# Kernel optimization log

Hardware: AMD Instinct MI355X
Metric: run time of the kernel (lower is better)

The kernel has to match this reference:

```python
import jax, jax.numpy as jnp
import numpy as np

N, F, E, WID, M, K = 100000, 128, 128, 4, 25000, 16
HID = WID * F    # width * num_features = 512
DHID = WID * E   # discriminator hidden = 512
EPS = 1e-5


def _v2v(x, v_idx, w_e):
    """Hypergraph v2v mean aggregation: v->e mean (scaled by w_e), then e->v mean."""
    Mm, Kk = v_idx.shape
    C = x.shape[1]
    ef = jnp.zeros((Mm, C), x.dtype)
    for k in range(Kk):  # K is small and static; avoids a [M,K,C] materialization
        ef = ef + x[v_idx[:, k]]
    ef = ef * (w_e / Kk)[:, None]  # weighted edge features [M, C]
    out = jnp.zeros_like(x)
    deg = jnp.zeros((x.shape[0],), x.dtype)
    for k in range(Kk):
        out = out.at[v_idx[:, k]].add(ef)
        deg = deg.at[v_idx[:, k]].add(1.0)
    return out / jnp.maximum(deg, 1.0)[:, None]


def _bn(h, g, bt):
    # BatchNorm1d in training mode: biased batch stats over vertex dim
    m = h.mean(0)
    v = ((h - m) ** 2).mean(0)
    return g * (h - m) * jax.lax.rsqrt(v + EPS) + bt


def _conv(x, Wt, b, g, bt, v_idx, w_e, last=False):
    h = _bn(x @ Wt.T + b, g, bt)
    h = _v2v(h, v_idx, w_e)
    return h if last else jax.nn.relu(h)  # dropout = identity (eval mode)


def setup_inputs() -> dict:
    key = jax.random.key(0)
    ks = iter(jax.random.split(key, 64))

    def lin(o, i):
        s = 1.0 / np.sqrt(i)
        return (jax.random.uniform(next(ks), (o, i), minval=-s, maxval=s, dtype=jnp.float32),
                jax.random.uniform(next(ks), (o,), minval=-s, maxval=s, dtype=jnp.float32))

    d = {}
    d["X"] = jax.random.normal(next(ks), (N, F), dtype=jnp.float32)
    d["v_idx"] = jax.random.randint(next(ks), (M, K), 0, N, dtype=jnp.int32)
    d["w_e"] = jax.random.uniform(next(ks), (M,), dtype=jnp.float32)
    for name, (o, i) in [("enc1", (HID, F)), ("enc2", (E, HID)), ("fc", (E, HID)),
                         ("f1u", (E, E)), ("f2u", (E, E)), ("f1r", (E, E)), ("f2r", (E, E)),
                         ("f1", (E, E)), ("f2", (E, E)),
                         ("dis1", (DHID, E)), ("dis2", (2, DHID)),
                         ("dec1", (HID, E)), ("dec2", (F, HID))]:
        Wt, b = lin(o, i)
        d[name + "_W"] = Wt
        d[name + "_b"] = b
    for name, c in [("enc1", HID), ("enc2", E), ("dis1", DHID), ("dis2", 2), ("dec1", HID), ("dec2", F)]:
        d[name + "_g"] = jnp.ones((c,), jnp.float32)
        d[name + "_bt"] = jnp.zeros((c,), jnp.float32)
    return d


def reference(X, v_idx, w_e,
              enc1_W, enc1_b, enc2_W, enc2_b, fc_W, fc_b,
              f1u_W, f1u_b, f2u_W, f2u_b, f1r_W, f1r_b, f2r_W, f2r_b,
              f1_W, f1_b, f2_W, f2_b,
              dis1_W, dis1_b, dis2_W, dis2_b, dec1_W, dec1_b, dec2_W, dec2_b,
              enc1_g, enc1_bt, enc2_g, enc2_bt, dis1_g, dis1_bt, dis2_g, dis2_bt,
              dec1_g, dec1_bt, dec2_g, dec2_bt):
    # encoder (returns last output and first-layer output)
    x1 = _conv(X, enc1_W, enc1_b, enc1_g, enc1_bt, v_idx, w_e)            # [N, HID]
    xe = _conv(x1, enc2_W, enc2_b, enc2_g, enc2_bt, v_idx, w_e, last=True)  # [N, E]
    xe1 = x1 @ fc_W.T + fc_b                                               # [N, E]
    # GRU-style gating
    z = jax.nn.sigmoid(xe1 @ f1u_W.T + f1u_b + xe @ f2u_W.T + f2u_b)
    r = jax.nn.sigmoid(xe1 @ f1r_W.T + f1r_b + xe @ f2r_W.T + f2r_b)
    o = jnp.tanh(xe1 @ f1_W.T + f1_b + (r * xe) @ f2_W.T + f2_b)
    outs = z * o + (1.0 - z) * xe                                          # [N, E]
    # attention pooling (n = input_size - 1)
    dd = (outs - outs.mean(0)) ** 2
    vv = dd.sum(0) / (N - 1)
    ee = dd / (4.0 * (vv + 0.001)) + 0.5
    proto = (outs * jax.nn.sigmoid(ee)).sum(0)                             # [E]
    # gradient reversal is identity in the forward pass
    h = _conv(outs, dis1_W, dis1_b, dis1_g, dis1_bt, v_idx, w_e)
    xdis = _conv(h, dis2_W, dis2_b, dis2_g, dis2_bt, v_idx, w_e, last=True)  # [N, 2]
    h = _conv(outs, dec1_W, dec1_b, dec1_g, dec1_bt, v_idx, w_e)
    x_de = _conv(h, dec2_W, dec2_b, dec2_g, dec2_bt, v_idx, w_e, last=True)  # [N, F]
    return (outs, x_de, proto, xdis)
```

## Files before the change

kernel.cpp:

```cpp
#include <hip/hip_runtime.h>
#include <cstddef>
#include <cstdint>

static constexpr int NV = 100000;
static constexpr int NP = 100096;
static constexpr int ME = 25000;
static constexpr int MEP = 25088;
static constexpr int KE = 16;
static constexpr float BN_EPS = 1e-5f;

typedef unsigned int u32;
typedef __attribute__((ext_vector_type(8))) short s16x8;
typedef __attribute__((ext_vector_type(8))) unsigned short u16x8;
typedef __attribute__((ext_vector_type(4))) float f32x4;

__device__ __forceinline__ float sigm(float x) { return 1.0f / (1.0f + expf(-x)); }
__device__ __forceinline__ float bf2f(unsigned short u) {
    union { u32 i; float f; } v; v.i = ((u32)u) << 16; return v.f;
}
__device__ __forceinline__ unsigned short f2bf(float f) {
    union { float f; u32 i; } v; v.f = f;
    u32 u = v.i;
    return (unsigned short)((u + 0x7FFFu + ((u >> 16) & 1u)) >> 16);
}

#define GLD16(g, l) __builtin_amdgcn_global_load_lds(                          \
    (__attribute__((address_space(1))) const unsigned int*)(g),                \
    (__attribute__((address_space(3))) unsigned int*)(l), 16, 0, 0)

#define STAGE_AB(b, k0)                                                        \
  {                                                                            \
    unsigned short* sA_ = sm + (b) * 12288;                                    \
    unsigned short* sB_ = sA_ + 8192;                                          \
    _Pragma("unroll")                                                          \
    for (int i_ = 0; i_ < 4; ++i_) {                                           \
      const unsigned short* g_ = A + (size_t)(bm + 32 * w + 8 * i_ + (l >> 3)) * IC + (k0) + swz; \
      GLD16(g_, sA_ + 2048 * w + 512 * i_);                                    \
    }                                                                          \
    _Pragma("unroll")                                                          \
    for (int i_ = 0; i_ < 2; ++i_) {                                           \
      const unsigned short* g_ = W + (size_t)(bn + 16 * w + 8 * i_ + (l >> 3)) * IC + (k0) + swz; \
      GLD16(g_, sB_ + 1024 * w + 512 * i_);                                    \
    }                                                                          \
  }

__global__ __launch_bounds__(256)
void mfma_gemm(const unsigned short* __restrict__ A, int IC,
               const unsigned short* __restrict__ W, const float* __restrict__ bias,
               unsigned short* __restrict__ Cb, int ldb, int cb0,
               unsigned short* __restrict__ Cb2, int ldb2, int splitN,
               float* __restrict__ s1f, float* __restrict__ s2f, int statsC)
{
    __shared__ unsigned short sm[2 * 12288];
    const int bm = blockIdx.y * 128;
    const int bn = blockIdx.x * 64;
    const int tid = threadIdx.x;
    const int l = tid & 63, w = tid >> 6;
    const int wrow = w >> 1, wcol = w & 1;

    f32x4 acc[4][2];
    #pragma unroll
    for (int m = 0; m < 4; ++m)
        #pragma unroll
        for (int n = 0; n < 2; ++n)
            #pragma unroll
            for (int r = 0; r < 4; ++r) acc[m][n][r] = 0.f;

    const int swz = (((l & 7) ^ (l >> 3)) << 3);
    const int nt = IC >> 6;

    STAGE_AB(0, 0);
    asm volatile("s_waitcnt vmcnt(0)" ::: "memory");
    __builtin_amdgcn_s_barrier();

    for (int t = 0; t < nt; ++t) {
        const int cur = t & 1;
        if (t + 1 < nt) STAGE_AB(cur ^ 1, (t + 1) << 6);
        const unsigned short* sA = sm + cur * 12288;
        const unsigned short* sB = sA + 8192;
        #pragma unroll
        for (int ks = 0; ks < 2; ++ks) {
            const int koff = ks * 32 + ((l >> 4) << 3);
            s16x8 afr[4], bfr[2];
            #pragma unroll
            for (int m = 0; m < 4; ++m) {
                int row = wrow * 64 + m * 16 + (l & 15);
                afr[m] = *(const s16x8*)&sA[row * 64 + (koff ^ ((l & 7) << 3))];
            }
            #pragma unroll
            for (int n = 0; n < 2; ++n) {
                int col = wcol * 32 + n * 16 + (l & 15);
                bfr[n] = *(const s16x8*)&sB[col * 64 + (koff ^ ((l & 7) << 3))];
            }
            #pragma unroll
            for (int m = 0; m < 4; ++m)
                #pragma unroll
                for (int n = 0; n < 2; ++n)
                    acc[m][n] = __builtin_amdgcn_mfma_f32_16x16x32_bf16(
                        afr[m], bfr[n], acc[m][n], 0, 0, 0);
        }
        asm volatile("s_waitcnt vmcnt(0)" ::: "memory");
        __builtin_amdgcn_s_barrier();
    }

    unsigned short* dst = Cb;
    int ld = ldb, co = cb0;
    if (Cb2 && bn >= splitN) { dst = Cb2; ld = ldb2; co = -splitN; }

    #pragma unroll
    for (int n = 0; n < 2; ++n) {
        const int col = bn + wcol * 32 + n * 16 + (l & 15);
        const float bs = bias[col];
        float ssum = 0.f, sq = 0.f;
        #pragma unroll
        for (int m = 0; m < 4; ++m) {
            const int row0 = bm + wrow * 64 + m * 16 + ((l >> 4) << 2);
            #pragma unroll
            for (int r = 0; r < 4; ++r) {
                float v = acc[m][n][r] + bs;
                int row = row0 + r;
                if (dst) dst[(size_t)row * ld + co + col] = f2bf(v);
                if (s1f && col < statsC && row < NV) { ssum += v; sq += v * v; }
            }
        }
        if (s1f && col < statsC) {
            ssum += __shfl_xor(ssum, 16); ssum += __shfl_xor(ssum, 32);
            sq   += __shfl_xor(sq, 16);   sq   += __shfl_xor(sq, 32);
            if ((l >> 4) == 0) {
                atomicAdd(&s1f[col], ssum);
                atomicAdd(&s2f[col], sq);
            }
        }
    }
}

__global__ __launch_bounds__(256)
void mfma_gemm_vtx(const unsigned short* __restrict__ A,
                   const unsigned short* __restrict__ W,
                   const float* __restrict__ P, const float* __restrict__ Q,
                   const float* __restrict__ sw,
                   unsigned short* __restrict__ dst, int ldd, int colStart,
                   const unsigned short* __restrict__ disW,
                   float* __restrict__ pre22)
{
    const int IC = 128;
    __shared__ unsigned short sm[2 * 12288];
    const int bm = blockIdx.y * 128;
    const int bn = blockIdx.x * 64;
    const int tid = threadIdx.x;
    const int l = tid & 63, w = tid >> 6;
    const int wrow = w >> 1, wcol = w & 1;

    f32x4 acc[4][2];
    #pragma unroll
    for (int m = 0; m < 4; ++m)
        #pragma unroll
        for (int n = 0; n < 2; ++n)
            #pragma unroll
            for (int r = 0; r < 4; ++r) acc[m][n][r] = 0.f;

    const int swz = (((l & 7) ^ (l >> 3)) << 3);

    STAGE_AB(0, 0);
    asm volatile("s_waitcnt vmcnt(0)" ::: "memory");
    __builtin_amdgcn_s_barrier();

    #pragma unroll
    for (int t = 0; t < 2; ++t) {
        const int cur = t & 1;
        if (t == 0) STAGE_AB(1, 64);
        const unsigned short* sA = sm + cur * 12288;
        const unsigned short* sB = sA + 8192;
        #pragma unroll
        for (int ks = 0; ks < 2; ++ks) {
            const int koff = ks * 32 + ((l >> 4) << 3);
            s16x8 afr[4], bfr[2];
            #pragma unroll
            for (int m = 0; m < 4; ++m) {
                int row = wrow * 64 + m * 16 + (l & 15);
                afr[m] = *(const s16x8*)&sA[row * 64 + (koff ^ ((l & 7) << 3))];
            }
            #pragma unroll
            for (int n = 0; n < 2; ++n) {
                int col = wcol * 32 + n * 16 + (l & 15);
                bfr[n] = *(const s16x8*)&sB[col * 64 + (koff ^ ((l & 7) << 3))];
            }
            #pragma unroll
            for (int m = 0; m < 4; ++m)
                #pragma unroll
                for (int n = 0; n < 2; ++n)
                    acc[m][n] = __builtin_amdgcn_mfma_f32_16x16x32_bf16(
                        afr[m], bfr[n], acc[m][n], 0, 0, 0);
        }
        asm volatile("s_waitcnt vmcnt(0)" ::: "memory");
        __builtin_amdgcn_s_barrier();
    }

    if (disW && bn < colStart) {
        #pragma unroll
        for (int m = 0; m < 4; ++m) {
            #pragma unroll
            for (int r = 0; r < 4; ++r) {
                const int row = bm + wrow * 64 + m * 16 + ((l >> 4) << 2) + r;
                const float swr = sw[row];
                float p0 = 0.f, p1 = 0.f;
                #pragma unroll
                for (int n = 0; n < 2; ++n) {
                    const int col = bn + wcol * 32 + n * 16 + (l & 15);
                    float h = fmaxf(P[col] * acc[m][n][r] + swr * Q[col], 0.f);
                    p0 += h * bf2f(disW[col]);
                    p1 += h * bf2f(disW[512 + col]);
                }
                p0 += __shfl_xor(p0, 1); p0 += __shfl_xor(p0, 2);
                p0 += __shfl_xor(p0, 4); p0 += __shfl_xor(p0, 8);
                p1 += __shfl_xor(p1, 1); p1 += __shfl_xor(p1, 2);
                p1 += __shfl_xor(p1, 4); p1 += __shfl_xor(p1, 8);
                if ((l & 15) == 0 && row < NV) {
                    atomicAdd(&pre22[2 * row], p0);
                    atomicAdd(&pre22[2 * row + 1], p1);
                }
            }
        }
    } else {
        #pragma unroll
        for (int n = 0; n < 2; ++n) {
            const int col = bn + wcol * 32 + n * 16 + (l & 15);
            const float pc = P[col], qc = Q[col];
            #pragma unroll
            for (int m = 0; m < 4; ++m) {
                const int row0 = bm + wrow * 64 + m * 16 + ((l >> 4) << 2);
                #pragma unroll
                for (int r = 0; r < 4; ++r) {
                    const int row = row0 + r;
                    float h = fmaxf(pc * acc[m][n][r] + sw[row] * qc, 0.f);
                    dst[(size_t)row * ldd + col - colStart] = f2bf(h);
                }
            }
        }
    }
}

__global__ __launch_bounds__(256)
void cov_kernel(const unsigned short* __restrict__ A, float* __restrict__ cov)
{
    __shared__ unsigned short T[128 * 64];
    const int tid = threadIdx.x;
    const int l = tid & 63, w = tid >> 6;

    f32x4 acc[2][8];
    #pragma unroll
    for (int m = 0; m < 2; ++m)
        #pragma unroll
        for (int n = 0; n < 8; ++n)
            #pragma unroll
            for (int r = 0; r < 4; ++r) acc[m][n][r] = 0.f;

    const int r0 = blockIdx.x * 1024;
    for (int ch = 0; ch < 16; ++ch) {
        const int rbase = r0 + ch * 64;
        __syncthreads();
        #pragma unroll
        for (int q = 0; q < 4; ++q) {
            int idx = tid + q * 256;
            int r = idx & 63, cg = idx >> 6;
            int row = rbase + r;
            u16x8 u = {0, 0, 0, 0, 0, 0, 0, 0};
            if (row < NV) u = *(const u16x8*)&A[(size_t)row * 128 + cg * 8];
            #pragma unroll
            for (int j = 0; j < 8; ++j) {
                int c = cg * 8 + j;
                T[c * 64 + (r ^ ((c & 7) << 3))] = u[j];
            }
        }
        __syncthreads();
        #pragma unroll
        for (int ks = 0; ks < 2; ++ks) {
            const int koff = ks * 32 + ((l >> 4) << 3);
            s16x8 fi[2], fj[8];
            #pragma unroll
            for (int m = 0; m < 2; ++m) {
                int c = (w * 2 + m) * 16 + (l & 15);
                fi[m] = *(const s16x8*)&T[c * 64 + (koff ^ ((c & 7) << 3))];
            }
            #pragma unroll
            for (int n = 0; n < 8; ++n) {
                int c = n * 16 + (l & 15);
                fj[n] = *(const s16x8*)&T[c * 64 + (koff ^ ((c & 7) << 3))];
            }
            #pragma unroll
            for (int m = 0; m < 2; ++m)
                #pragma unroll
                for (int n = 0; n < 8; ++n)
                    acc[m][n] = __builtin_amdgcn_mfma_f32_16x16x32_bf16(
                        fi[m], fj[n], acc[m][n], 0, 0, 0);
        }
    }
    #pragma unroll
    for (int m = 0; m < 2; ++m) {
        #pragma unroll
        for (int n = 0; n < 8; ++n) {
            #pragma unroll
            for (int r = 0; r < 4; ++r) {
                int row = (w * 2 + m) * 16 + ((l >> 4) << 2) + r;
                int col = n * 16 + (l & 15);
                atomicAdd(&cov[row * 128 + col], acc[m][n][r]);
            }
        }
    }
}

__global__ __launch_bounds__(128)
void quadform_kernel(const float* __restrict__ cov, const float* __restrict__ colsum,
                     const unsigned short* __restrict__ Wt, const float* __restrict__ bias,
                     float* __restrict__ s1, float* __restrict__ s2)
{
    const int c = blockIdx.x, i = threadIdx.x;
    __shared__ float wv[128];
    __shared__ float red[128][2];
    float wi = bf2f(Wt[c * 128 + i]);
    wv[i] = wi;
    __syncthreads();
    const float* crow = cov + i * 128;
    float dot = 0.f;
    #pragma unroll 8
    for (int j = 0; j < 128; ++j) dot += crow[j] * wv[j];
    red[i][0] = wi * dot;
    red[i][1] = wi * colsum[i];
    __syncthreads();
    for (int s = 64; s > 0; s >>= 1) {
        if (i < s) { red[i][0] += red[i + s][0]; red[i][1] += red[i + s][1]; }
        __syncthreads();
    }
    if (i == 0) {
        float b = bias[c];
        float ws = red[0][1];
        s1[c] = ws + (float)NV * b;
        s2[c] = red[0][0] + 2.f * b * ws + (float)NV * b * b;
    }
}

__global__ void prep_weights(const float* e1, const float* e2, const float* fcw,
                             const float* d1, const float* dc1, const float* dc2,
                             const float* ds2,
                             const float* f1u, const float* f2u,
                             const float* f1r, const float* f2r,
                             const float* f1, const float* f2,
                             const float* f1ub, const float* f2ub,
                             const float* f1rb, const float* f2rb,
                             const float* f1b, const float* f2b,
                             const float* ds1b, const float* dc1b,
                             const float* e2b, const float* fcb,
                             unsigned short* WB, float* bzr, float* bo,
                             float* bdd, float* bef)
{
    int i = blockIdx.x * 256 + threadIdx.x;
    if (i < 65536)           WB[i] = f2bf(e1[i]);
    else if (i < 131072)     WB[i] = f2bf(e2[i - 65536]);
    else if (i < 196608)     WB[i] = f2bf(fcw[i - 131072]);
    else if (i < 262144)     WB[i] = f2bf(d1[i - 196608]);
    else if (i < 327680)     WB[i] = f2bf(dc1[i - 262144]);
    else if (i < 393216)     WB[i] = f2bf(dc2[i - 327680]);
    else if (i < 394240)     WB[i] = f2bf(ds2[i - 393216]);
    else if (i < 459776) {
        int j = i - 394240, row = j >> 8, c = j & 255;
        float v;
        if (row < 128) v = (c < 128) ? f1u[row * 128 + c] : f2u[row * 128 + c - 128];
        else { int rr = row - 128; v = (c < 128) ? f1r[rr * 128 + c] : f2r[rr * 128 + c - 128]; }
        WB[i] = f2bf(v);
    } else if (i < 492544) {
        int j = i - 459776, row = j >> 8, c = j & 255;
        float v = (c < 128) ? f1[row * 128 + c] : f2[row * 128 + c - 128];
        WB[i] = f2bf(v);
    } else if (i < 492800) {
        int o = i - 492544;
        bzr[o] = (o < 128) ? (f1ub[o] + f2ub[o]) : (f1rb[o - 128] + f2rb[o - 128]);
    } else if (i < 492928) {
        int o = i - 492800;
        bo[o] = f1b[o] + f2b[o];
    } else if (i < 493952) {
        int o = i - 492928;
        bdd[o] = (o < 512) ? ds1b[o] : dc1b[o - 512];
    } else if (i < 494208) {
        int o = i - 493952;
        bef[o] = (o < 128) ? e2b[o] : fcb[o - 128];
    }
}

__global__ void cvt_f32_bf16(const float* __restrict__ in, unsigned short* __restrict__ out, int n)
{
    int i = (blockIdx.x * 256 + threadIdx.x) * 4;
    if (i < n) {
        float4 v = *reinterpret_cast<const float4*>(&in[i]);
        out[i] = f2bf(v.x); out[i + 1] = f2bf(v.y);
        out[i + 2] = f2bf(v.z); out[i + 3] = f2bf(v.w);
    }
}

__global__ void bn_finalize_kernel(const float* __restrict__ s1, const float* __restrict__ s2,
                                   const float* __restrict__ g, const float* __restrict__ bt,
                                   float* __restrict__ scale, float* __restrict__ shift,
                                   int C, float invN)
{
    int c = threadIdx.x;
    if (c < C) {
        float m = s1[c] * invN;
        float v = fmaxf(s2[c] * invN - m * m, 0.f);
        float sc = g[c] * rsqrtf(v + BN_EPS);
        scale[c] = sc;
        shift[c] = bt[c] - m * sc;
    }
}

__global__ void bn_finalize_pq(const float* __restrict__ s1, const float* __restrict__ s2,
                               const float* __restrict__ g, const float* __restrict__ bt,
                               const float* __restrict__ bias,
                               float* __restrict__ P, float* __restrict__ Q,
                               int C, int off, float invN)
{
    int c = threadIdx.x;
    if (c < C) {
        int cc = off + c;
        float m = s1[cc] * invN;
        float v = fmaxf(s2[cc] * invN - m * m, 0.f);
        float sc = g[c] * rsqrtf(v + BN_EPS);
        float sh = bt[c] - m * sc;
        P[cc] = sc;
        Q[cc] = sc * bias[c] + sh;
    }
}

__global__ __launch_bounds__(256)
void edge_gather_sum(const unsigned short* __restrict__ x, const int* __restrict__ vidx,
                     unsigned short* __restrict__ ge)
{
    const int e = blockIdx.x * 16 + (threadIdx.x >> 4);
    const int cp = (threadIdx.x & 15) << 3;
    if (e >= ME) return;
    float s[8] = {};
    const int* vi = vidx + e * KE;
    #pragma unroll
    for (int k = 0; k < KE; ++k) {
        int v = vi[k];
        u16x8 u = *(const u16x8*)&x[(size_t)v * 128 + cp];
        #pragma unroll
        for (int j = 0; j < 8; ++j) s[j] += bf2f(u[j]);
    }
    u16x8 o;
    #pragma unroll
    for (int j = 0; j < 8; ++j) o[j] = f2bf(s[j]);
    *(u16x8*)&ge[(size_t)e * 128 + cp] = o;
}

__global__ __launch_bounds__(256)
void csr_gather_g2(const unsigned short* __restrict__ ge, const float* __restrict__ we,
                   const int* __restrict__ rowptr, const int* __restrict__ csr,
                   unsigned short* __restrict__ g2, float* __restrict__ swv)
{
    const int v = blockIdx.x * 16 + (threadIdx.x >> 4);
    const int lg = threadIdx.x & 15;
    if (v >= NP) return;
    if (v >= NV) {
        u16x8 z = {0, 0, 0, 0, 0, 0, 0, 0};
        *(u16x8*)&g2[(size_t)v * 128 + lg * 8] = z;
        if (swv && lg == 0) swv[v] = 0.f;
        return;
    }
    const int s = rowptr[v], e = rowptr[v + 1];
    float a[8] = {};
    float ws = 0.f;
    for (int i = s; i < e; ++i) {
        int ed = csr[i];
        float wt = we[ed];
        ws += wt;
        u16x8 u = *(const u16x8*)&ge[(size_t)ed * 128 + lg * 8];
        #pragma unroll
        for (int j = 0; j < 8; ++j) a[j] = fmaf(wt, bf2f(u[j]), a[j]);
    }
    float inv = 1.0f / (float)max(e - s, 1);
    float invK = inv * (1.0f / KE);
    u16x8 o;
    #pragma unroll
    for (int j = 0; j < 8; ++j) o[j] = f2bf(a[j] * invK);
    *(u16x8*)&g2[(size_t)v * 128 + lg * 8] = o;
    if (swv && lg == 0) swv[v] = ws * inv;
}

__global__ __launch_bounds__(256)
void edge_gather_bf(const unsigned short* __restrict__ pre, const int* __restrict__ vidx,
                    const float* __restrict__ we, const float* __restrict__ scl,
                    const float* __restrict__ shf, unsigned short* __restrict__ ef, int C)
{
    const int tpe = C >> 3;
    const int epb = 256 / tpe;
    const int e = blockIdx.x * epb + threadIdx.x / tpe;
    const int cp = (threadIdx.x % tpe) << 3;
    if (e >= ME) return;
    float s[8] = {};
    const int* vi = vidx + e * KE;
    #pragma unroll
    for (int k = 0; k < KE; ++k) {
        int v = vi[k];
        u16x8 u = *(const u16x8*)&pre[(size_t)v * C + cp];
        #pragma unroll
        for (int j = 0; j < 8; ++j) s[j] += bf2f(u[j]);
    }
    float wv = we[e] * (1.0f / KE);
    u16x8 o;
    #pragma unroll
    for (int j = 0; j < 8; ++j)
        o[j] = f2bf(wv * (scl[cp + j] * s[j] + (float)KE * shf[cp + j]));
    *(u16x8*)&ef[(size_t)e * C + cp] = o;
}

__global__ void edge_gather2_kernel(const float* __restrict__ X, const int* __restrict__ vidx,
                                    const float* __restrict__ we, const float* __restrict__ scale,
                                    const float* __restrict__ shift, float* __restrict__ ef)
{
    int e = blockIdx.x * blockDim.x + threadIdx.x;
    if (e >= ME) return;
    float s0 = 0.f, s1v = 0.f;
    #pragma unroll
    for (int k = 0; k < KE; ++k) {
        int v = vidx[e * KE + k];
        s0 += X[2 * v];
        s1v += X[2 * v + 1];
    }
    float w = we[e] * (1.0f / KE);
    ef[2 * e]     = w * (scale[0] * s0 + (float)KE * shift[0]);
    ef[2 * e + 1] = w * (scale[1] * s1v + (float)KE * shift[1]);
}

__global__ void deg_kernel(const int* __restrict__ vidx, int* __restrict__ deg)
{
    int i = blockIdx.x * blockDim.x + threadIdx.x;
    if (i < ME * KE) atomicAdd(&deg[vidx[i]], 1);
}

__global__ void scan_block_kernel(const int* __restrict__ deg, int* __restrict__ rowptr,
                                  int* __restrict__ blocksums, int n)
{
    __shared__ int tmp[256];
    int i = blockIdx.x * 256 + threadIdx.x;
    int v = (i < n) ? deg[i] : 0;
    tmp[threadIdx.x] = v;
    __syncthreads();
    for (int off = 1; off < 256; off <<= 1) {
        int t = (threadIdx.x >= off) ? tmp[threadIdx.x - off] : 0;
        __syncthreads();
        tmp[threadIdx.x] += t;
        __syncthreads();
    }
    if (i < n) rowptr[i] = tmp[threadIdx.x] - v;
    if (threadIdx.x == 255) blocksums[blockIdx.x] = tmp[255];
}

__global__ void scan_sums_par(int* __restrict__ bs, int nb)
{
    __shared__ int tmp[512];
    int t = threadIdx.x;
    int v = (t < nb) ? bs[t] : 0;
    tmp[t] = v;
    __syncthreads();
    for (int off = 1; off < 512; off <<= 1) {
        int u = (t >= off) ? tmp[t - off] : 0;
        __syncthreads();
        tmp[t] += u;
        __syncthreads();
    }
    if (t < nb) bs[t] = tmp[t] - v;
}

__global__ void scan_add_kernel(int* __restrict__ rowptr, const int* __restrict__ blocksums, int n)
{
    int i = blockIdx.x * 256 + threadIdx.x;
    if (i < n) rowptr[i] += blocksums[blockIdx.x];
    if (i == 0) rowptr[n] = ME * KE;
}

__global__ void csr_fill_kernel(const int* __restrict__ vidx, int* __restrict__ cursor,
                                int* __restrict__ csr)
{
    int i = blockIdx.x * blockDim.x + threadIdx.x;
    if (i < ME * KE) {
        int v = vidx[i];
        int pos = atomicAdd(&cursor[v], 1);
        csr[pos] = i >> 4;
    }
}

__global__ __launch_bounds__(256)
void csr_gather_bf(const unsigned short* __restrict__ ef, int ldE, int cb0E,
                   const int* __restrict__ rowptr, const int* __restrict__ csr,
                   float* __restrict__ outf, int ldf,
                   unsigned short* __restrict__ outb, int ldb, int cb0,
                   unsigned short* __restrict__ outb2, int ldb2,
                   int C, int relu)
{
    const int lpv = C >> 3;
    const int vpb = 256 / lpv;
    const int v = blockIdx.x * vpb + threadIdx.x / lpv;
    const int lg = threadIdx.x % lpv;
    if (v >= NV) return;
    const int s = rowptr[v], e = rowptr[v + 1];
    float a[8] = {};
    int i = s;
    for (; i + 2 <= e; i += 2) {
        int e0 = csr[i], e1 = csr[i + 1];
        u16x8 u0 = *(const u16x8*)&ef[(size_t)e0 * ldE + cb0E + lg * 8];
        u16x8 u1 = *(const u16x8*)&ef[(size_t)e1 * ldE + cb0E + lg * 8];
        #pragma unroll
        for (int j = 0; j < 8; ++j) a[j] += bf2f(u0[j]) + bf2f(u1[j]);
    }
    if (i < e) {
        int e0 = csr[i];
        u16x8 u0 = *(const u16x8*)&ef[(size_t)e0 * ldE + cb0E + lg * 8];
        #pragma unroll
        for (int j = 0; j < 8; ++j) a[j] += bf2f(u0[j]);
    }
    float inv = 1.0f / (float)max(e - s, 1);
    #pragma unroll
    for (int j = 0; j < 8; ++j) {
        float x = a[j] * inv;
        if (relu) x = fmaxf(x, 0.f);
        a[j] = x;
    }
    if (outf) {
        float* p = outf + (size_t)v * ldf + lg * 8;
        #pragma unroll
        for (int j = 0; j < 8; ++j) p[j] = a[j];
    }
    if (outb) {
        u16x8 o;
        #pragma unroll
        for (int j = 0; j < 8; ++j) o[j] = f2bf(a[j]);
        *(u16x8*)&outb[(size_t)v * ldb + cb0 + lg * 8] = o;
    }
    if (outb2) {
        u16x8 o;
        #pragma unroll
        for (int j = 0; j < 8; ++j) o[j] = f2bf(a[j]);
        *(u16x8*)&outb2[(size_t)v * ldb2 + lg * 8] = o;
    }
}

__global__ void csr_gather2_kernel(const float* __restrict__ ef, const int* __restrict__ rowptr,
                                   const int* __restrict__ csr, float* __restrict__ outp)
{
    int v = blockIdx.x * blockDim.x + threadIdx.x;
    if (v >= NV) return;
    int s = rowptr[v], e = rowptr[v + 1];
    float a0 = 0.f, a1 = 0.f;
    for (int i = s; i < e; ++i) {
        int ed = csr[i];
        a0 += ef[2 * ed];
        a1 += ef[2 * ed + 1];
    }
    float inv = 1.0f / (float)max(e - s, 1);
    outp[2 * v]     = a0 * inv;
    outp[2 * v + 1] = a1 * inv;
}

__global__ __launch_bounds__(256)
void colstats_bf(const unsigned short* __restrict__ Xb,
                 float* __restrict__ s1, float* __restrict__ s2)
{
    const int t = threadIdx.x;
    const int cg = t & 15;
    const int rs = t >> 4;
    float s[8] = {}, q[8] = {};
    for (int r = blockIdx.x * 16 + rs; r < NV; r += 256 * 16) {
        u16x8 u = *(const u16x8*)&Xb[(size_t)r * 128 + cg * 8];
        #pragma unroll
        for (int j = 0; j < 8; ++j) {
            float v = bf2f(u[j]);
            s[j] += v; q[j] += v * v;
        }
    }
    __shared__ float ls[16][16][8];
    __shared__ float lq[16][16][8];
    #pragma unroll
    for (int j = 0; j < 8; ++j) { ls[rs][cg][j] = s[j]; lq[rs][cg][j] = q[j]; }
    __syncthreads();
    int c = t & 127;
    float a = 0.f;
    if (t < 128) {
        #pragma unroll
        for (int i = 0; i < 16; ++i) a += ls[i][c >> 3][c & 7];
        atomicAdd(&s1[c], a);
    } else {
        #pragma unroll
        for (int i = 0; i < 16; ++i) a += lq[i][c >> 3][c & 7];
        atomicAdd(&s2[c], a);
    }
}

__global__ void att_finalize_kernel(const float* __restrict__ s1, const float* __restrict__ s2,
                                    float* __restrict__ mu, float* __restrict__ qd, int C)
{
    int c = threadIdx.x;
    if (c < C) {
        float m = s1[c] / (float)NV;
        float vv = fmaxf((s2[c] - (float)NV * m * m) / (float)(NV - 1), 0.f);
        mu[c] = m;
        qd[c] = 1.0f / (4.0f * (vv + 0.001f));
    }
}

__global__ __launch_bounds__(256)
void proto_ws(const float* __restrict__ outsf, const float* __restrict__ mu,
              const float* __restrict__ qd, float* __restrict__ proto)
{
    const int t = threadIdx.x;
    const int cg = t & 31;
    const int rs = t >> 5;
    const float4* X4 = (const float4*)outsf;
    const float4 m = ((const float4*)mu)[cg];
    const float4 q = ((const float4*)qd)[cg];
    float4 acc = make_float4(0.f, 0.f, 0.f, 0.f);
    for (int r = blockIdx.x * 8 + rs; r < NV; r += 256 * 8) {
        float4 x = X4[(size_t)r * 32 + cg];
        float d0 = (x.x - m.x) * (x.x - m.x);
        float d1 = (x.y - m.y) * (x.y - m.y);
        float d2 = (x.z - m.z) * (x.z - m.z);
        float d3 = (x.w - m.w) * (x.w - m.w);
        acc.x += x.x * sigm(d0 * q.x + 0.5f);
        acc.y += x.y * sigm(d1 * q.y + 0.5f);
        acc.z += x.z * sigm(d2 * q.z + 0.5f);
        acc.w += x.w * sigm(d3 * q.w + 0.5f);
    }
    __shared__ float4 ls[8][32];
    ls[rs][cg] = acc;
    __syncthreads();
    if (t < 128) {
        float a = 0.f;
        #pragma unroll
        for (int i = 0; i < 8; ++i) {
            const float* f = (const float*)&ls[i][t >> 2];
            a += f[t & 3];
        }
        atomicAdd(&proto[t], a);
    }
}

__global__ void colstats2_kernel(const float* __restrict__ X, int N,
                                 float* __restrict__ s1, float* __restrict__ s2)
{
    __shared__ float red[256][4];
    int t = threadIdx.x;
    float a0 = 0, a1 = 0, b0 = 0, b1 = 0;
    for (int r = blockIdx.x * 256 + t; r < N; r += 256 * gridDim.x) {
        float x0 = X[2 * r], x1 = X[2 * r + 1];
        a0 += x0; b0 += x0 * x0;
        a1 += x1; b1 += x1 * x1;
    }
    red[t][0] = a0; red[t][1] = a1; red[t][2] = b0; red[t][3] = b1;
    __syncthreads();
    for (int s = 128; s > 0; s >>= 1) {
        if (t < s)
            for (int j = 0; j < 4; ++j) red[t][j] += red[t + s][j];
        __syncthreads();
    }
    if (t == 0) {
        atomicAdd(&s1[0], red[0][0]);
        atomicAdd(&s1[1], red[0][1]);
        atomicAdd(&s2[0], red[0][2]);
        atomicAdd(&s2[1], red[0][3]);
    }
}

__global__ void rx_kernel(const unsigned short* __restrict__ ZR, const unsigned short* __restrict__ xeb,
                          unsigned short* __restrict__ G, int n8)
{
    int idx = blockIdx.x * blockDim.x + threadIdx.x;
    if (idx >= n8) return;
    int i8 = idx * 8;
    int row = i8 >> 7, c = i8 & 127;
    u16x8 rv = *(const u16x8*)&ZR[(size_t)row * 256 + 128 + c];
    u16x8 xv = *(const u16x8*)&xeb[i8];
    u16x8 g;
    #pragma unroll
    for (int j = 0; j < 8; ++j)
        g[j] = f2bf(sigm(bf2f(rv[j])) * bf2f(xv[j]));
    *(u16x8*)&G[(size_t)row * 256 + 128 + c] = g;
}

__global__ void gru_out_kernel(const unsigned short* __restrict__ ZR, const unsigned short* __restrict__ Opre,
                               const unsigned short* __restrict__ xeb,
                               float* __restrict__ outs, unsigned short* __restrict__ outsb,
                               float* __restrict__ outsf, int n8)
{
    int idx = blockIdx.x * blockDim.x + threadIdx.x;
    if (idx >= n8) return;
    int i8 = idx * 8;
    int row = i8 >> 7, c = i8 & 127;
    u16x8 zv = *(const u16x8*)&ZR[(size_t)row * 256 + c];
    u16x8 ov = *(const u16x8*)&Opre[i8];
    u16x8 xv = *(const u16x8*)&xeb[i8];
    float val[8];
    u16x8 ob;
    #pragma unroll
    for (int j = 0; j < 8; ++j) {
        float z = sigm(bf2f(zv[j]));
        float o = tanhf(bf2f(ov[j]));
        float xe = bf2f(xv[j]);
        val[j] = z * o + (1.f - z) * xe;
        ob[j] = f2bf(val[j]);
    }
    *(float4*)&outs[i8]     = make_float4(val[0], val[1], val[2], val[3]);
    *(float4*)&outs[i8 + 4] = make_float4(val[4], val[5], val[6], val[7]);
    *(float4*)&outsf[i8]     = make_float4(val[0], val[1], val[2], val[3]);
    *(float4*)&outsf[i8 + 4] = make_float4(val[4], val[5], val[6], val[7]);
    *(u16x8*)&outsb[i8] = ob;
}

extern "C" void kernel_launch(void* const* d_in, const int* in_sizes, int n_in,
                              void* d_out, int out_size, void* d_ws, size_t ws_size,
                              hipStream_t stream)
{
    const float* X      = (const float*)d_in[0];
    const int*   vidx   = (const int*)  d_in[1];
    const float* we     = (const float*)d_in[2];
    const float* enc1_W = (const float*)d_in[3];  const float* enc1_b = (const float*)d_in[4];
    const float* enc2_W = (const float*)d_in[5];  const float* enc2_b = (const float*)d_in[6];
    const float* fc_W   = (const float*)d_in[7];  const float* fc_b   = (const float*)d_in[8];
    const float* f1u_W  = (const float*)d_in[9];  const float* f1u_b  = (const float*)d_in[10];
    const float* f2u_W  = (const float*)d_in[11]; const float* f2u_b  = (const float*)d_in[12];
    const float* f1r_W  = (const float*)d_in[13]; const float* f1r_b  = (const float*)d_in[14];
    const float* f2r_W  = (const float*)d_in[15]; const float* f2r_b  = (const float*)d_in[16];
    const float* f1_W   = (const float*)d_in[17]; const float* f1_b   = (const float*)d_in[18];
    const float* f2_W   = (const float*)d_in[19]; const float* f2_b   = (const float*)d_in[20];
    const float* dis1_W = (const float*)d_in[21]; const float* dis1_b = (const float*)d_in[22];
    const float* dis2_W = (const float*)d_in[23]; const float* dis2_b = (const float*)d_in[24];
    const float* dec1_W = (const float*)d_in[25]; const float* dec1_b = (const float*)d_in[26];
    const float* dec2_W = (const float*)d_in[27]; const float* dec2_b = (const float*)d_in[28];
    const float* enc1_g = (const float*)d_in[29]; const float* enc1_bt = (const float*)d_in[30];
    const float* enc2_g = (const float*)d_in[31]; const float* enc2_bt = (const float*)d_in[32];
    const float* dis1_g = (const float*)d_in[33]; const float* dis1_bt = (const float*)d_in[34];
    const float* dis2_g = (const float*)d_in[35]; const float* dis2_bt = (const float*)d_in[36];
    const float* dec1_g = (const float*)d_in[37]; const float* dec1_bt = (const float*)d_in[38];
    const float* dec2_g = (const float*)d_in[39]; const float* dec2_bt = (const float*)d_in[40];

    float* out   = (float*)d_out;
    float* outs  = out;
    float* x_de  = out + 12800000;
    float* proto = out + 25600000;
    float* xdis  = out + 25600128;

    char* base = (char*)d_ws;
    unsigned short* bufA = (unsigned short*)base;
    char* p = base + (size_t)NP * 512 * 2;
    unsigned short* bufE = (unsigned short*)p; p += (size_t)MEP * 1024 * 2;
    unsigned short* Greg = (unsigned short*)p;
    unsigned short* Xbf  = Greg;
    unsigned short* outsb = Greg + (size_t)NP * 128;
    p += (size_t)NP * 256 * 2;
    unsigned short* x1bf = (unsigned short*)p; p += (size_t)NP * 512 * 2;
    unsigned short* WB = (unsigned short*)p; p += 492544 * 2 + 1024;
    float* bzr = (float*)p; p += 256 * 4;
    float* bo  = (float*)p; p += 128 * 4;
    float* bdd = (float*)p; p += 1024 * 4;
    float* bef = (float*)p; p += 256 * 4;
    float* s1  = (float*)p; p += 1024 * 4;
    float* s2  = (float*)p; p += 1024 * 4;
    float* scl = (float*)p; p += 1024 * 4;
    float* shf = (float*)p; p += 1024 * 4;
    float* sX1 = (float*)p; p += 128 * 4;
    float* sX2 = (float*)p; p += 128 * 4;
    float* sA1 = (float*)p; p += 128 * 4;
    float* sA2 = (float*)p; p += 128 * 4;
    float* covX = (float*)p; p += 16384 * 4;
    float* covA = (float*)p; p += 16384 * 4;
    int* deg    = (int*)p; p += (size_t)NV * 4;
    int* rowptr = (int*)p; p += (size_t)(NV + 1) * 4;
    int* cursor = (int*)p; p += (size_t)NV * 4;
    int* bsums  = (int*)p; p += 512 * 4;
    int* csr    = (int*)p; p += (size_t)ME * KE * 4;
    float* outsf = (float*)p; p += (size_t)NP * 128 * 4;
    unsigned short* ge = (unsigned short*)p; p += (size_t)MEP * 128 * 2;
    float* sw = (float*)p;

    unsigned short* g2 = bufE + (size_t)MEP * 128;

    unsigned short* pre128 = bufA;
    unsigned short* xe_bf  = bufA + (size_t)NP * 128;
    unsigned short* ZR     = bufA + (size_t)NP * 256;
    unsigned short* Opre   = bufA;
    unsigned short* hdec   = bufA;
    float* pre22 = (float*)(Greg + (size_t)NP * 128);
    float* bufEf = (float*)bufE;

    unsigned short* wenc1 = WB;
    unsigned short* wenc2 = WB + 65536;
    unsigned short* wdd   = WB + 196608;
    unsigned short* wdec2 = WB + 327680;
    unsigned short* wdis2 = WB + 393216;
    unsigned short* wzr   = WB + 394240;
    unsigned short* wo    = WB + 459776;

    const int n128 = NV * 128;
    const int n8 = n128 / 8;
    const int nScanBlocks = (NV + 255) / 256;

    auto gemm = [&](const unsigned short* A, int ic, const unsigned short* W, const float* b,
                    unsigned short* Cb, int ldb, int cb0,
                    unsigned short* Cb2, int ldb2, int splitN,
                    int oc, float* st1, float* st2, int statsC) {
        dim3 g(oc / 64, NP / 128);
        mfma_gemm<<<g, 256, 0, stream>>>(A, ic, W, b, Cb, ldb, cb0, Cb2, ldb2, splitN,
                                         st1, st2, statsC);
    };

    prep_weights<<<1931, 256, 0, stream>>>(enc1_W, enc2_W, fc_W, dis1_W, dec1_W, dec2_W, dis2_W,
                                           f1u_W, f2u_W, f1r_W, f2r_W, f1_W, f2_W,
                                           f1u_b, f2u_b, f1r_b, f2r_b, f1_b, f2_b,
                                           dis1_b, dec1_b, enc2_b, fc_b,
                                           WB, bzr, bo, bdd, bef);
    cvt_f32_bf16<<<(n128 / 4 + 255) / 256, 256, 0, stream>>>(X, Xbf, n128);

    hipMemsetAsync(deg, 0, NV * sizeof(int), stream);
    deg_kernel<<<(ME * KE + 255) / 256, 256, 0, stream>>>(vidx, deg);
    scan_block_kernel<<<nScanBlocks, 256, 0, stream>>>(deg, rowptr, bsums, NV);
    scan_sums_par<<<1, 512, 0, stream>>>(bsums, nScanBlocks);
    scan_add_kernel<<<nScanBlocks, 256, 0, stream>>>(rowptr, bsums, NV);
    hipMemcpyAsync(cursor, rowptr, NV * sizeof(int), hipMemcpyDeviceToDevice, stream);
    csr_fill_kernel<<<(ME * KE + 255) / 256, 256, 0, stream>>>(vidx, cursor, csr);

    hipMemsetAsync(sX1, 0, 256 * sizeof(float), stream);
    hipMemsetAsync(covX, 0, 16384 * sizeof(float), stream);
    colstats_bf<<<256, 256, 0, stream>>>(Xbf, sX1, sX2);
    cov_kernel<<<98, 256, 0, stream>>>(Xbf, covX);
    quadform_kernel<<<512, 128, 0, stream>>>(covX, sX1, wenc1, enc1_b, s1, s2);
    bn_finalize_pq<<<1, 512, 0, stream>>>(s1, s2, enc1_g, enc1_bt, enc1_b, scl, shf, 512, 0, 1.0f / NV);
    edge_gather_sum<<<(ME + 15) / 16, 256, 0, stream>>>(Xbf, vidx, ge);
    csr_gather_g2<<<NP / 16, 256, 0, stream>>>(ge, we, rowptr, csr, g2, sw);
    { dim3 g(8, NP / 128);
      mfma_gemm_vtx<<<g, 256, 0, stream>>>(g2, wenc1, scl, shf, sw, x1bf, 512, 0,
                                           nullptr, nullptr); }

    hipMemsetAsync(s1, 0, 2048 * sizeof(float), stream);
    gemm(x1bf, 512, wenc2, bef, pre128, 128, 0, Greg, 256, 128, 256, s1, s2, 128);
    bn_finalize_kernel<<<1, 512, 0, stream>>>(s1, s2, enc2_g, enc2_bt, scl, shf, 128, 1.0f / NV);
    edge_gather_bf<<<(ME + 15) / 16, 256, 0, stream>>>(pre128, vidx, we, scl, shf, bufE, 128);
    csr_gather_bf<<<NV / 16, 256, 0, stream>>>(bufE, 128, 0, rowptr, csr,
        nullptr, 0, Greg, 256, 128, xe_bf, 128, 128, 0);

    gemm(Greg, 256, wzr, bzr, ZR, 256, 0, nullptr, 0, 1 << 30, 256, nullptr, nullptr, 0);
    rx_kernel<<<(n8 + 255) / 256, 256, 0, stream>>>(ZR, xe_bf, Greg, n8);
    gemm(Greg, 256, wo, bo, Opre, 128, 0, nullptr, 0, 1 << 30, 128, nullptr, nullptr, 0);
    gru_out_kernel<<<(n8 + 255) / 256, 256, 0, stream>>>(ZR, Opre, xe_bf, outs, outsb, outsf, n8);

    hipMemsetAsync(sA1, 0, 256 * sizeof(float), stream);
    colstats_bf<<<256, 256, 0, stream>>>(outsb, sA1, sA2);
    att_finalize_kernel<<<1, 128, 0, stream>>>(sA1, sA2, scl, shf, 128);
    hipMemsetAsync(proto, 0, 128 * sizeof(float), stream);
    proto_ws<<<256, 256, 0, stream>>>(outsf, scl, shf, proto);

    hipMemsetAsync(covA, 0, 16384 * sizeof(float), stream);
    cov_kernel<<<98, 256, 0, stream>>>(outsb, covA);
    quadform_kernel<<<1024, 128, 0, stream>>>(covA, sA1, wdd, bdd, s1, s2);
    bn_finalize_pq<<<1, 512, 0, stream>>>(s1, s2, dis1_g, dis1_bt, dis1_b, scl, shf, 512, 0, 1.0f / NV);
    bn_finalize_pq<<<1, 512, 0, stream>>>(s1, s2, dec1_g, dec1_bt, dec1_b, scl, shf, 512, 512, 1.0f / NV);
    edge_gather_sum<<<(ME + 15) / 16, 256, 0, stream>>>(outsb, vidx, ge);
    csr_gather_g2<<<NP / 16, 256, 0, stream>>>(ge, we, rowptr, csr, g2, nullptr);
    hipMemsetAsync(pre22, 0, (size_t)NV * 2 * sizeof(float), stream);
    { dim3 g(16, NP / 128);
      mfma_gemm_vtx<<<g, 256, 0, stream>>>(g2, wdd, scl, shf, sw, hdec, 512, 512,
                                           wdis2, pre22); }

    hipMemsetAsync(s1, 0, 2048 * sizeof(float), stream);
    colstats2_kernel<<<64, 256, 0, stream>>>(pre22, NV, s1, s2);
    bn_finalize_kernel<<<1, 512, 0, stream>>>(s1, s2, dis2_g, dis2_bt, scl, shf, 2, 1.0f / NV);
    edge_gather2_kernel<<<(ME + 255) / 256, 256, 0, stream>>>(pre22, vidx, we, scl, shf, bufEf);
    csr_gather2_kernel<<<(NV + 255) / 256, 256, 0, stream>>>(bufEf, rowptr, csr, xdis);

    hipMemsetAsync(s1, 0, 2048 * sizeof(float), stream);
    gemm(hdec, 512, wdec2, dec2_b, Greg, 128, 0, nullptr, 0, 1 << 30, 128, s1, s2, 128);
    bn_finalize_kernel<<<1, 512, 0, stream>>>(s1, s2, dec2_g, dec2_bt, scl, shf, 128, 1.0f / NV);
    edge_gather_bf<<<(ME + 15) / 16, 256, 0, stream>>>(Greg, vidx, we, scl, shf, bufE, 128);
    csr_gather_bf<<<NV / 16, 256, 0, stream>>>(bufE, 128, 0, rowptr, csr,
        x_de, 128, nullptr, 0, 0, nullptr, 0, 128, 0);
}
```

Measured before the change: 938.8 us.

## Read GEMM weights directly from global, widen vtx tiles, replace atomics with partial-sum reduce

The GEMM kernels no longer stage the weight (B) tile in LDS; B fragments are loaded straight from global memory (the small weights stay cache-resident), which halves LDS use and removes the B staging loads. The vertex GEMM is widened to 128 output columns per block, halving the grid and reusing each A tile across more columns. The dis2 projection no longer uses per-row float atomics. It writes per-slice float2 partials that a new reduce22 kernel sums, which also removes a memset. The risk is uncoalesced global B reads in the inner loop and more accumulator registers per thread.

Measured after the change: 906.3 us. 1.04x faster.

```diff
diff --git a/kernel.cpp b/kernel.cpp
--- a/kernel.cpp
+++ b/kernel.cpp
@@ -28,19 +28,13 @@
     (__attribute__((address_space(1))) const unsigned int*)(g),                \
     (__attribute__((address_space(3))) unsigned int*)(l), 16, 0, 0)
 
-#define STAGE_AB(b, k0)                                                        \
+#define STAGE_A(b, k0)                                                         \
   {                                                                            \
-    unsigned short* sA_ = sm + (b) * 12288;                                    \
-    unsigned short* sB_ = sA_ + 8192;                                          \
+    unsigned short* sA_ = sm + (b) * 8192;                                     \
     _Pragma("unroll")                                                          \
     for (int i_ = 0; i_ < 4; ++i_) {                                           \
       const unsigned short* g_ = A + (size_t)(bm + 32 * w + 8 * i_ + (l >> 3)) * IC + (k0) + swz; \
       GLD16(g_, sA_ + 2048 * w + 512 * i_);                                    \
-    }                                                                          \
-    _Pragma("unroll")                                                          \
-    for (int i_ = 0; i_ < 2; ++i_) {                                           \
-      const unsigned short* g_ = W + (size_t)(bn + 16 * w + 8 * i_ + (l >> 3)) * IC + (k0) + swz; \
-      GLD16(g_, sB_ + 1024 * w + 512 * i_);                                    \
     }                                                                          \
   }
 
@@ -51,7 +45,7 @@
                unsigned short* __restrict__ Cb2, int ldb2, int splitN,
                float* __restrict__ s1f, float* __restrict__ s2f, int statsC)
 {
-    __shared__ unsigned short sm[2 * 12288];
+    __shared__ unsigned short sm[2 * 8192];
     const int bm = blockIdx.y * 128;
     const int bn = blockIdx.x * 64;
     const int tid = threadIdx.x;
@@ -69,15 +63,14 @@
     const int swz = (((l & 7) ^ (l >> 3)) << 3);
     const int nt = IC >> 6;
 
-    STAGE_AB(0, 0);
+    STAGE_A(0, 0);
     asm volatile("s_waitcnt vmcnt(0)" ::: "memory");
     __builtin_amdgcn_s_barrier();
 
     for (int t = 0; t < nt; ++t) {
         const int cur = t & 1;
-        if (t + 1 < nt) STAGE_AB(cur ^ 1, (t + 1) << 6);
-        const unsigned short* sA = sm + cur * 12288;
-        const unsigned short* sB = sA + 8192;
+        if (t + 1 < nt) STAGE_A(cur ^ 1, (t + 1) << 6);
+        const unsigned short* sA = sm + cur * 8192;
         #pragma unroll
         for (int ks = 0; ks < 2; ++ks) {
             const int koff = ks * 32 + ((l >> 4) << 3);
@@ -89,8 +82,8 @@
             }
             #pragma unroll
             for (int n = 0; n < 2; ++n) {
-                int col = wcol * 32 + n * 16 + (l & 15);
-                bfr[n] = *(const s16x8*)&sB[col * 64 + (koff ^ ((l & 7) << 3))];
+                int col = bn + wcol * 32 + n * 16 + (l & 15);
+                bfr[n] = *(const s16x8*)&W[(size_t)col * IC + (t << 6) + koff];
             }
             #pragma unroll
             for (int m = 0; m < 4; ++m)
@@ -135,60 +128,60 @@
 }
 
 __global__ __launch_bounds__(256)
-void mfma_gemm_vtx(const unsigned short* __restrict__ A,
-                   const unsigned short* __restrict__ W,
-                   const float* __restrict__ P, const float* __restrict__ Q,
-                   const float* __restrict__ sw,
-                   unsigned short* __restrict__ dst, int ldd, int colStart,
-                   const unsigned short* __restrict__ disW,
-                   float* __restrict__ pre22)
+void mfma_gemm_vtx2(const unsigned short* __restrict__ A,
+                    const unsigned short* __restrict__ W,
+                    const float* __restrict__ P, const float* __restrict__ Q,
+                    const float* __restrict__ sw,
+                    unsigned short* __restrict__ dst, int ldd, int colStart,
+                    int disCols, const unsigned short* __restrict__ disW,
+                    float2* __restrict__ pre22p)
 {
     const int IC = 128;
-    __shared__ unsigned short sm[2 * 12288];
+    __shared__ unsigned short sm[2 * 8192];
     const int bm = blockIdx.y * 128;
-    const int bn = blockIdx.x * 64;
+    const int bx = blockIdx.x;
+    const int bn0 = bx * 128;
     const int tid = threadIdx.x;
     const int l = tid & 63, w = tid >> 6;
     const int wrow = w >> 1, wcol = w & 1;
 
-    f32x4 acc[4][2];
+    f32x4 acc[4][4];
     #pragma unroll
     for (int m = 0; m < 4; ++m)
         #pragma unroll
-        for (int n = 0; n < 2; ++n)
+        for (int n = 0; n < 4; ++n)
             #pragma unroll
             for (int r = 0; r < 4; ++r) acc[m][n][r] = 0.f;
 
     const int swz = (((l & 7) ^ (l >> 3)) << 3);
 
-    STAGE_AB(0, 0);
+    STAGE_A(0, 0);
     asm volatile("s_waitcnt vmcnt(0)" ::: "memory");
     __builtin_amdgcn_s_barrier();
 
     #pragma unroll
     for (int t = 0; t < 2; ++t) {
         const int cur = t & 1;
-        if (t == 0) STAGE_AB(1, 64);
-        const unsigned short* sA = sm + cur * 12288;
-        const unsigned short* sB = sA + 8192;
+        if (t == 0) STAGE_A(1, 64);
+        const unsigned short* sA = sm + cur * 8192;
         #pragma unroll
         for (int ks = 0; ks < 2; ++ks) {
             const int koff = ks * 32 + ((l >> 4) << 3);
-            s16x8 afr[4], bfr[2];
+            s16x8 afr[4], bfr[4];
             #pragma unroll
             for (int m = 0; m < 4; ++m) {
                 int row = wrow * 64 + m * 16 + (l & 15);
                 afr[m] = *(const s16x8*)&sA[row * 64 + (koff ^ ((l & 7) << 3))];
             }
             #pragma unroll
-            for (int n = 0; n < 2; ++n) {
-                int col = wcol * 32 + n * 16 + (l & 15);
-                bfr[n] = *(const s16x8*)&sB[col * 64 + (koff ^ ((l & 7) << 3))];
+            for (int n = 0; n < 4; ++n) {
+                int colg = bn0 + wcol * 64 + n * 16 + (l & 15);
+                bfr[n] = *(const s16x8*)&W[(size_t)colg * 128 + (t << 6) + koff];
             }
             #pragma unroll
             for (int m = 0; m < 4; ++m)
                 #pragma unroll
-                for (int n = 0; n < 2; ++n)
+                for (int n = 0; n < 4; ++n)
                     acc[m][n] = __builtin_amdgcn_mfma_f32_16x16x32_bf16(
                         afr[m], bfr[n], acc[m][n], 0, 0, 0);
         }
@@ -196,36 +189,43 @@
         __builtin_amdgcn_s_barrier();
     }
 
-    if (disW && bn < colStart) {
+    if (bn0 < disCols) {
+        float pc[4], qc[4], w0f[4], w1f[4];
+        #pragma unroll
+        for (int n = 0; n < 4; ++n) {
+            int colg = bn0 + wcol * 64 + n * 16 + (l & 15);
+            pc[n] = P[colg]; qc[n] = Q[colg];
+            w0f[n] = bf2f(disW[colg]);
+            w1f[n] = bf2f(disW[512 + colg]);
+        }
+        const int slice = bx * 2 + wcol;
         #pragma unroll
         for (int m = 0; m < 4; ++m) {
+            const int row0 = bm + wrow * 64 + m * 16 + ((l >> 4) << 2);
             #pragma unroll
             for (int r = 0; r < 4; ++r) {
-                const int row = bm + wrow * 64 + m * 16 + ((l >> 4) << 2) + r;
+                const int row = row0 + r;
                 const float swr = sw[row];
                 float p0 = 0.f, p1 = 0.f;
                 #pragma unroll
-                for (int n = 0; n < 2; ++n) {
-                    const int col = bn + wcol * 32 + n * 16 + (l & 15);
-                    float h = fmaxf(P[col] * acc[m][n][r] + swr * Q[col], 0.f);
-                    p0 += h * bf2f(disW[col]);
-                    p1 += h * bf2f(disW[512 + col]);
+                for (int n = 0; n < 4; ++n) {
+                    float h = fmaxf(pc[n] * acc[m][n][r] + swr * qc[n], 0.f);
+                    p0 += h * w0f[n];
+                    p1 += h * w1f[n];
                 }
                 p0 += __shfl_xor(p0, 1); p0 += __shfl_xor(p0, 2);
                 p0 += __shfl_xor(p0, 4); p0 += __shfl_xor(p0, 8);
                 p1 += __shfl_xor(p1, 1); p1 += __shfl_xor(p1, 2);
                 p1 += __shfl_xor(p1, 4); p1 += __shfl_xor(p1, 8);
-                if ((l & 15) == 0 && row < NV) {
-                    atomicAdd(&pre22[2 * row], p0);
-                    atomicAdd(&pre22[2 * row + 1], p1);
-                }
+                if ((l & 15) == 0)
+                    pre22p[(size_t)slice * NP + row] = make_float2(p0, p1);
             }
         }
     } else {
         #pragma unroll
-        for (int n = 0; n < 2; ++n) {
-            const int col = bn + wcol * 32 + n * 16 + (l & 15);
-            const float pc = P[col], qc = Q[col];
+        for (int n = 0; n < 4; ++n) {
+            const int colg = bn0 + wcol * 64 + n * 16 + (l & 15);
+            const float pc = P[colg], qc = Q[colg];
             #pragma unroll
             for (int m = 0; m < 4; ++m) {
                 const int row0 = bm + wrow * 64 + m * 16 + ((l >> 4) << 2);
@@ -233,11 +233,25 @@
                 for (int r = 0; r < 4; ++r) {
                     const int row = row0 + r;
                     float h = fmaxf(pc * acc[m][n][r] + sw[row] * qc, 0.f);
-                    dst[(size_t)row * ldd + col - colStart] = f2bf(h);
+                    dst[(size_t)row * ldd + colg - colStart] = f2bf(h);
                 }
             }
         }
     }
+}
+
+__global__ void reduce22(const float2* __restrict__ p, float* __restrict__ pre22)
+{
+    int v = blockIdx.x * 256 + threadIdx.x;
+    if (v >= NV) return;
+    float a = 0.f, b = 0.f;
+    #pragma unroll
+    for (int s = 0; s < 8; ++s) {
+        float2 t = p[(size_t)s * NP + v];
+        a += t.x; b += t.y;
+    }
+    pre22[2 * v] = a;
+    pre22[2 * v + 1] = b;
 }
 
 __global__ __launch_bounds__(256)
@@ -880,6 +894,7 @@
     float* sw = (float*)p;
 
     unsigned short* g2 = bufE + (size_t)MEP * 128;
+    float2* pre22p = (float2*)(bufE + (size_t)MEP * 128 + (size_t)NP * 128);
 
     unsigned short* pre128 = bufA;
     unsigned short* xe_bf  = bufA + (size_t)NP * 128;
@@ -933,9 +948,9 @@
     bn_finalize_pq<<<1, 512, 0, stream>>>(s1, s2, enc1_g, enc1_bt, enc1_b, scl, shf, 512, 0, 1.0f / NV);
     edge_gather_sum<<<(ME + 15) / 16, 256, 0, stream>>>(Xbf, vidx, ge);
     csr_gather_g2<<<NP / 16, 256, 0, stream>>>(ge, we, rowptr, csr, g2, sw);
-    { dim3 g(8, NP / 128);
-      mfma_gemm_vtx<<<g, 256, 0, stream>>>(g2, wenc1, scl, shf, sw, x1bf, 512, 0,
-                                           nullptr, nullptr); }
+    { dim3 g(4, NP / 128);
+      mfma_gemm_vtx2<<<g, 256, 0, stream>>>(g2, wenc1, scl, shf, sw, x1bf, 512, 0,
+                                            0, nullptr, nullptr); }
 
     hipMemsetAsync(s1, 0, 2048 * sizeof(float), stream);
     gemm(x1bf, 512, wenc2, bef, pre128, 128, 0, Greg, 256, 128, 256, s1, s2, 128);
@@ -962,10 +977,10 @@
     bn_finalize_pq<<<1, 512, 0, stream>>>(s1, s2, dec1_g, dec1_bt, dec1_b, scl, shf, 512, 512, 1.0f / NV);
     edge_gather_sum<<<(ME + 15) / 16, 256, 0, stream>>>(outsb, vidx, ge);
     csr_gather_g2<<<NP / 16, 256, 0, stream>>>(ge, we, rowptr, csr, g2, nullptr);
-    hipMemsetAsync(pre22, 0, (size_t)NV * 2 * sizeof(float), stream);
-    { dim3 g(16, NP / 128);
-      mfma_gemm_vtx<<<g, 256, 0, stream>>>(g2, wdd, scl, shf, sw, hdec, 512, 512,
-                                           wdis2, pre22); }
+    { dim3 g(8, NP / 128);
+      mfma_gemm_vtx2<<<g, 256, 0, stream>>>(g2, wdd, scl, shf, sw, hdec, 512, 512,
+                                            512, wdis2, pre22p); }
+    reduce22<<<(NV + 255) / 256, 256, 0, stream>>>(pre22p, pre22);
 
     hipMemsetAsync(s1, 0, 2048 * sizeof(float), stream);
     colstats2_kernel<<<64, 256, 0, stream>>>(pre22, NV, s1, s2);
```
